# Performance work log

Hardware: AMD Instinct MI355X
Metric: run time of the kernel (lower is better)

Reference implementation:

```python
import jax, jax.numpy as jnp
import numpy as np

D = 512        # feat_dim
H_ENC = 8      # motion_encoder heads
H_SA = 4       # semantic-aware attention heads
BS, L, N = 8, 512, 4096
LN_EPS = 1e-5


def _layernorm(x, g, b):
    m = jnp.mean(x, axis=-1, keepdims=True)
    v = jnp.var(x, axis=-1, keepdims=True)
    return (x - m) * jax.lax.rsqrt(v + LN_EPS) * g + b


def _linear(x, w, b):
    # torch nn.Linear convention: w [out, in]
    return x @ w.T + b


def setup_inputs() -> dict:
    key = jax.random.key(0)
    ks = jax.random.split(key, 24)
    s = 0.02
    inp = {
        "motion": jax.random.normal(ks[0], (BS, L, D), jnp.float32),
        "scene_xyz": jax.random.normal(ks[1], (BS, N, 3), jnp.float32),
        "scene_feats": jax.random.normal(ks[2], (BS, N, D), jnp.float32),
        "spatial_prior": jax.random.normal(ks[3], (BS, L, N), jnp.float32),
        # motion_encoder (pre-norm MHA + pre-norm MLP, both residual)
        "enc_ln1_g": jnp.ones((D,), jnp.float32),
        "enc_ln1_b": jnp.zeros((D,), jnp.float32),
        "enc_qkv_w": jax.random.normal(ks[4], (3 * D, D), jnp.float32) * s,
        "enc_qkv_b": jnp.zeros((3 * D,), jnp.float32),
        "enc_out_w": jax.random.normal(ks[5], (D, D), jnp.float32) * s,
        "enc_out_b": jnp.zeros((D,), jnp.float32),
        "enc_ln2_g": jnp.ones((D,), jnp.float32),
        "enc_ln2_b": jnp.zeros((D,), jnp.float32),
        "enc_ff1_w": jax.random.normal(ks[6], (D, D), jnp.float32) * s,
        "enc_ff1_b": jnp.zeros((D,), jnp.float32),
        "enc_ff2_w": jax.random.normal(ks[7], (D, D), jnp.float32) * s,
        "enc_ff2_b": jnp.zeros((D,), jnp.float32),
        # SemanticAwareAttention
        "sa_q_w": jax.random.normal(ks[8], (D, D), jnp.float32) * s,
        "sa_q_b": jnp.zeros((D,), jnp.float32),
        "sa_kv_w": jax.random.normal(ks[9], (2 * D, D), jnp.float32) * s,
        "sa_kv_b": jnp.zeros((2 * D,), jnp.float32),
        "sa_out_w": jax.random.normal(ks[10], (D, D), jnp.float32) * s,
        "sa_out_b": jnp.zeros((D,), jnp.float32),
        # final concat-MLP: in 2D -> 4D -> D  (Mlp(2D, D, expansion=4))
        "mlp_fc1_w": jax.random.normal(ks[11], (4 * D, 2 * D), jnp.float32) * s,
        "mlp_fc1_b": jnp.zeros((4 * D,), jnp.float32),
        "mlp_fc2_w": jax.random.normal(ks[12], (D, 4 * D), jnp.float32) * s,
        "mlp_fc2_b": jnp.zeros((D,), jnp.float32),
    }
    return inp


def _forward(motion, scene_xyz, scene_feats, spatial_prior,
             enc_ln1_g, enc_ln1_b, enc_qkv_w, enc_qkv_b, enc_out_w, enc_out_b,
             enc_ln2_g, enc_ln2_b, enc_ff1_w, enc_ff1_b, enc_ff2_w, enc_ff2_b,
             sa_q_w, sa_q_b, sa_kv_w, sa_kv_b, sa_out_w, sa_out_b,
             mlp_fc1_w, mlp_fc1_b, mlp_fc2_w, mlp_fc2_b):
    bs, slen, _ = motion.shape
    n = scene_feats.shape[1]
    dh_enc = D // H_ENC
    dh_sa = D // H_SA

    # ---- motion encoder: pre-norm MHA + residual ----
    h = _layernorm(motion, enc_ln1_g, enc_ln1_b)
    qkv = _linear(h, enc_qkv_w, enc_qkv_b)                      # [bs, L, 3D]
    q, k, v = jnp.split(qkv, 3, axis=-1)
    q = q.reshape(bs, slen, H_ENC, dh_enc)
    k = k.reshape(bs, slen, H_ENC, dh_enc)
    v = v.reshape(bs, slen, H_ENC, dh_enc)
    att = jnp.einsum("bqhd,bkhd->bhqk", q, k) * (dh_enc ** -0.5)
    att = jax.nn.softmax(att, axis=-1)
    o = jnp.einsum("bhqk,bkhd->bqhd", att, v).reshape(bs, slen, D)
    x = motion + _linear(o, enc_out_w, enc_out_b)

    # ---- pre-norm MLP + residual ----
    h2 = _layernorm(x, enc_ln2_g, enc_ln2_b)
    ff = _linear(jax.nn.gelu(_linear(h2, enc_ff1_w, enc_ff1_b), approximate=False),
                 enc_ff2_w, enc_ff2_b)
    motion_sca = x + ff

    # ---- SemanticAwareAttention ----
    q = _linear(motion_sca, sa_q_w, sa_q_b) * (D ** -0.5)       # scale by feat_dim (faithful)
    kv = _linear(scene_feats, sa_kv_w, sa_kv_b)
    k, v = jnp.split(kv, 2, axis=-1)
    # faithful to torch: q.view(bs, H, L, d) splits heads from flattened (L, D)
    q = q.reshape(bs, H_SA, slen, dh_sa)
    k = k.reshape(bs, n, H_SA, dh_sa).transpose(0, 2, 1, 3)     # [bs, H, N, d]
    v = v.reshape(bs, n, H_SA, dh_sa).transpose(0, 2, 1, 3)
    att = jnp.einsum("bhqd,bhkd->bhqk", q, k) + spatial_prior[:, None, :, :]
    att = jax.nn.softmax(att, axis=-1)
    sm = jnp.einsum("bhqk,bhkd->bqhd", att, v).reshape(bs, slen, D)
    sm_feature = _linear(sm, sa_out_w, sa_out_b)

    # ---- concat + MLP ----
    cat = jnp.concatenate([motion_sca, sm_feature], axis=-1)    # [bs, L, 2D]
    out = _linear(jax.nn.gelu(_linear(cat, mlp_fc1_w, mlp_fc1_b), approximate=False),
                  mlp_fc2_w, mlp_fc2_b)
    return out


def reference(motion, scene_xyz, scene_feats, spatial_prior,
              enc_ln1_g, enc_ln1_b, enc_qkv_w, enc_qkv_b, enc_out_w, enc_out_b,
              enc_ln2_g, enc_ln2_b, enc_ff1_w, enc_ff1_b, enc_ff2_w, enc_ff2_b,
              sa_q_w, sa_q_b, sa_kv_w, sa_kv_b, sa_out_w, sa_out_b,
              mlp_fc1_w, mlp_fc1_b, mlp_fc2_w, mlp_fc2_b):
    return _forward(motion, scene_xyz, scene_feats, spatial_prior,
                    enc_ln1_g, enc_ln1_b, enc_qkv_w, enc_qkv_b, enc_out_w, enc_out_b,
                    enc_ln2_g, enc_ln2_b, enc_ff1_w, enc_ff1_b, enc_ff2_w, enc_ff2_b,
                    sa_q_w, sa_q_b, sa_kv_w, sa_kv_b, sa_out_w, sa_out_b,
                    mlp_fc1_w, mlp_fc1_b, mlp_fc2_w, mlp_fc2_b)
```

## Files before the change

### kernel.cpp

```cpp
#include <hip/hip_runtime.h>

typedef unsigned short bf16_t;
typedef __attribute__((ext_vector_type(8))) short bf16x8;
typedef __attribute__((ext_vector_type(4))) float f32x4;

__device__ __forceinline__ float bf2f(bf16_t u) {
  union { unsigned int i; float f; } v; v.i = ((unsigned int)u) << 16; return v.f;
}
__device__ __forceinline__ bf16_t f2bf(float f) {
  union { float f; unsigned int i; } v; v.f = f;
  unsigned int u = v.i;
  u += 0x7fffu + ((u >> 16) & 1u);
  return (bf16_t)(u >> 16);
}
__device__ __forceinline__ float gelu_exact(float x) {
  return 0.5f * x * (1.0f + erff(x * 0.7071067811865475f));
}
__device__ __forceinline__ void g2l16(bf16_t* l, const bf16_t* g) {
  __builtin_amdgcn_global_load_lds(
      (const __attribute__((address_space(1))) unsigned int*)g,
      (__attribute__((address_space(3))) unsigned int*)l, 16, 0, 0);
}

__global__ __launch_bounds__(256) void f2bf_kernel(const float4* __restrict__ s,
                                                   ushort4* __restrict__ d, int n4) {
  int i = blockIdx.x * 256 + threadIdx.x;
  if (i < n4) {
    float4 f = s[i];
    ushort4 u; u.x = f2bf(f.x); u.y = f2bf(f.y); u.z = f2bf(f.z); u.w = f2bf(f.w);
    d[i] = u;
  }
}

__global__ __launch_bounds__(256) void ln_kernel(const float* __restrict__ x,
                                                 const float* __restrict__ g,
                                                 const float* __restrict__ bta,
                                                 bf16_t* __restrict__ y) {
  const int w = threadIdx.x >> 6, lane = threadIdx.x & 63;
  const long row = (long)blockIdx.x * 4 + w;
  const long base = row * 512;
  const int c0 = lane << 2;
  float v[8];
  float4 f0 = *(const float4*)(x + base + c0);
  float4 f1 = *(const float4*)(x + base + 256 + c0);
  v[0]=f0.x; v[1]=f0.y; v[2]=f0.z; v[3]=f0.w;
  v[4]=f1.x; v[5]=f1.y; v[6]=f1.z; v[7]=f1.w;
  float s = 0.f;
#pragma unroll
  for (int c=0;c<8;++c) s += v[c];
#pragma unroll
  for (int o=32;o>0;o>>=1) s += __shfl_xor(s, o);
  const float mean = s * 0.001953125f;
  float ss = 0.f;
#pragma unroll
  for (int c=0;c<8;++c) { float d = v[c]-mean; ss += d*d; }
#pragma unroll
  for (int o=32;o>0;o>>=1) ss += __shfl_xor(ss, o);
  const float rstd = rsqrtf(ss * 0.001953125f + 1e-5f);
  ushort4 o0, o1;
  o0.x = f2bf((v[0]-mean)*rstd*g[c0+0] + bta[c0+0]);
  o0.y = f2bf((v[1]-mean)*rstd*g[c0+1] + bta[c0+1]);
  o0.z = f2bf((v[2]-mean)*rstd*g[c0+2] + bta[c0+2]);
  o0.w = f2bf((v[3]-mean)*rstd*g[c0+3] + bta[c0+3]);
  o1.x = f2bf((v[4]-mean)*rstd*g[256+c0+0] + bta[256+c0+0]);
  o1.y = f2bf((v[5]-mean)*rstd*g[256+c0+1] + bta[256+c0+1]);
  o1.z = f2bf((v[6]-mean)*rstd*g[256+c0+2] + bta[256+c0+2]);
  o1.w = f2bf((v[7]-mean)*rstd*g[256+c0+3] + bta[256+c0+3]);
  *(ushort4*)(y + base + c0) = o0;
  *(ushort4*)(y + base + 256 + c0) = o1;
}

struct MmaNT {
  const bf16_t* A; const bf16_t* W; const float* bias; const float* res; void* C;
  long lda, sAb, sAh;
  long ldw, sWb, sWh;
  long ldr, sRb, sRh;
  long ldc, sCb, sCh;
  int K, zdiv, cBf, act;
  float scale;
};

template <int MT>
__global__ __launch_bounds__(256) void mma_nt_kernel(MmaNT p) {
  constexpr int FM = MT / 32;
  constexpr int TILE_E = (MT + 128) * 32;
  constexpr int ST_E = MT * 128;
  constexpr int SM_E = (TILE_E > ST_E) ? TILE_E : ST_E;
  __shared__ __align__(16) bf16_t smem[SM_E];
  bf16_t* Al = smem;
  bf16_t* Wl = smem + MT * 32;
  const int tid = threadIdx.x;
  const int wid = tid >> 6, lane = tid & 63;
  const int wm = wid & 1, wn = wid >> 1;
  const int quad = lane >> 4, l16 = lane & 15;
  const int z = blockIdx.z;
  const int zb = z / p.zdiv, zh = z % p.zdiv;

  const int nbx = gridDim.x;
  const int nwg = nbx * gridDim.y;
  const int flat = blockIdx.y * nbx + blockIdx.x;
  const int sw = (flat & 7) * (nwg >> 3) + (flat >> 3);
  const int bx = sw % nbx, by = sw / nbx;

  const long m0 = (long)by * MT;
  const long n0 = (long)bx * 128;

  f32x4 zero4 = {0.f, 0.f, 0.f, 0.f};
  f32x4 acc[FM][4];
#pragma unroll
  for (int fm = 0; fm < FM; ++fm)
#pragma unroll
    for (int fn = 0; fn < 4; ++fn) acc[fm][fn] = zero4;

  if constexpr (MT == 128) {
    const bf16_t* Ag = p.A + (long)zb * p.sAb + (long)zh * p.sAh + m0 * p.lda;
    const bf16_t* Wg = p.W + (long)zb * p.sWb + (long)zh * p.sWh + n0 * p.ldw;
    const int sr = lane >> 2;
    const int sc = (lane & 3) * 8;
    for (int kc = 0; kc < p.K; kc += 32) {
#pragma unroll
      for (int j = 0; j < 2; ++j)
        g2l16(&Al[(j * 64 + wid * 16) * 32],
              Ag + (long)(j * 64 + wid * 16 + sr) * p.lda + kc + sc);
#pragma unroll
      for (int j = 0; j < 2; ++j)
        g2l16(&Wl[(j * 64 + wid * 16) * 32],
              Wg + (long)(j * 64 + wid * 16 + sr) * p.ldw + kc + sc);
      __syncthreads();
      bf16x8 af[FM], wf[4];
#pragma unroll
      for (int fm = 0; fm < FM; ++fm)
        af[fm] = *(const bf16x8*)&Al[(wm * 64 + fm * 16 + l16) * 32 + quad * 8];
#pragma unroll
      for (int fn = 0; fn < 4; ++fn)
        wf[fn] = *(const bf16x8*)&Wl[(wn * 64 + fn * 16 + l16) * 32 + quad * 8];
#pragma unroll
      for (int fm = 0; fm < FM; ++fm)
#pragma unroll
        for (int fn = 0; fn < 4; ++fn)
          acc[fm][fn] = __builtin_amdgcn_mfma_f32_16x16x32_bf16(af[fm], wf[fn], acc[fm][fn], 0, 0, 0);
      __syncthreads();
    }
  } else {
    const bf16_t* Ag = p.A + (long)zb * p.sAb + (long)zh * p.sAh +
                       (m0 + wm * (MT / 2) + l16) * p.lda;
    const bf16_t* Wg = p.W + (long)zb * p.sWb + (long)zh * p.sWh +
                       (n0 + wn * 64 + l16) * p.ldw;
    bf16x8 a0[FM], w0[4], a1[FM], w1[4], an0[FM], wn0[4], an1[FM], wn1[4];
#pragma unroll
    for (int fm = 0; fm < FM; ++fm) {
      a0[fm] = *(const bf16x8*)(Ag + (long)(fm * 16) * p.lda + quad * 8);
      a1[fm] = *(const bf16x8*)(Ag + (long)(fm * 16) * p.lda + 32 + quad * 8);
    }
#pragma unroll
    for (int fn = 0; fn < 4; ++fn) {
      w0[fn] = *(const bf16x8*)(Wg + (long)(fn * 16) * p.ldw + quad * 8);
      w1[fn] = *(const bf16x8*)(Wg + (long)(fn * 16) * p.ldw + 32 + quad * 8);
    }
    for (int kc = 0; kc < p.K; kc += 64) {
      int k2 = kc + 64;
      if (k2 > p.K - 64) k2 = p.K - 64;
#pragma unroll
      for (int fm = 0; fm < FM; ++fm)
        an0[fm] = *(const bf16x8*)(Ag + (long)(fm * 16) * p.lda + k2 + quad * 8);
#pragma unroll
      for (int fn = 0; fn < 4; ++fn)
        wn0[fn] = *(const bf16x8*)(Wg + (long)(fn * 16) * p.ldw + k2 + quad * 8);
#pragma unroll
      for (int fm = 0; fm < FM; ++fm)
#pragma unroll
        for (int fn = 0; fn < 4; ++fn)
          acc[fm][fn] = __builtin_amdgcn_mfma_f32_16x16x32_bf16(a0[fm], w0[fn], acc[fm][fn], 0, 0, 0);
#pragma unroll
      for (int fm = 0; fm < FM; ++fm)
        an1[fm] = *(const bf16x8*)(Ag + (long)(fm * 16) * p.lda + k2 + 32 + quad * 8);
#pragma unroll
      for (int fn = 0; fn < 4; ++fn)
        wn1[fn] = *(const bf16x8*)(Wg + (long)(fn * 16) * p.ldw + k2 + 32 + quad * 8);
#pragma unroll
      for (int fm = 0; fm < FM; ++fm)
#pragma unroll
        for (int fn = 0; fn < 4; ++fn)
          acc[fm][fn] = __builtin_amdgcn_mfma_f32_16x16x32_bf16(a1[fm], w1[fn], acc[fm][fn], 0, 0, 0);
#pragma unroll
      for (int fm = 0; fm < FM; ++fm) { a0[fm] = an0[fm]; a1[fm] = an1[fm]; }
#pragma unroll
      for (int fn = 0; fn < 4; ++fn) { w0[fn] = wn0[fn]; w1[fn] = wn1[fn]; }
    }
  }

  const long cOff = (long)zb * p.sCb + (long)zh * p.sCh;
  const long rOff = (long)zb * p.sRb + (long)zh * p.sRh;
  if (p.cBf) {
#pragma unroll
    for (int fm = 0; fm < FM; ++fm) {
#pragma unroll
      for (int fn = 0; fn < 4; ++fn) {
        const int lc = wn * 64 + fn * 16 + l16;
        const long col = n0 + lc;
        const float bv = p.bias ? p.bias[col] : 0.f;
#pragma unroll
        for (int r = 0; r < 4; ++r) {
          const int lr = wm * (MT / 2) + fm * 16 + quad * 4 + r;
          float t = acc[fm][fn][r] + bv;
          if (p.act) t = gelu_exact(t);
          t *= p.scale;
          if (p.res) t += p.res[rOff + (m0 + lr) * p.ldr + col];
          smem[lr * 128 + lc] = f2bf(t);
        }
      }
    }
    __syncthreads();
    bf16_t* Cg = (bf16_t*)p.C + cOff + m0 * p.ldc + n0;
#pragma unroll
    for (int i = 0; i < MT / 16; ++i) {
      const int flat2 = tid + i * 256;
      const int r = flat2 >> 4, c = (flat2 & 15) * 8;
      *(uint4*)(Cg + (long)r * p.ldc + c) = *(const uint4*)&smem[r * 128 + c];
    }
  } else {
#pragma unroll
    for (int fm = 0; fm < FM; ++fm) {
#pragma unroll
      for (int fn = 0; fn < 4; ++fn) {
        const long col = n0 + wn * 64 + fn * 16 + l16;
        const float bv = p.bias ? p.bias[col] : 0.f;
#pragma unroll
        for (int r = 0; r < 4; ++r) {
          const long row = m0 + wm * (MT / 2) + fm * 16 + quad * 4 + r;
          float t = acc[fm][fn][r] + bv;
          if (p.act) t = gelu_exact(t);
          t *= p.scale;
          if (p.res) t += p.res[rOff + row * p.ldr + col];
          ((float*)p.C)[cOff + row * p.ldc + col] = t;
        }
      }
    }
  }
}

struct TransP {
  const bf16_t* src; bf16_t* dst;
  long sSb, sSh, ld;
  int nh, N, D;
};

__global__ __launch_bounds__(256) void transpose_kernel(TransP p) {
  __shared__ bf16_t T[64][72];
  const int tid = threadIdx.x;
  const int z = blockIdx.z;
  const int zb = z / p.nh, zh = z % p.nh;
  const long n0 = (long)blockIdx.x * 64;
  const long d0 = (long)blockIdx.y * 64;
  const bf16_t* src = p.src + (long)zb * p.sSb + (long)zh * p.sSh;
  bf16_t* dst = p.dst + (long)z * p.D * p.N;
#pragma unroll
  for (int i = 0; i < 2; ++i) {
    int flat = tid + i * 256, r = flat >> 3, cg = flat & 7;
    uint4 v = *(const uint4*)(src + (n0 + r) * p.ld + d0 + cg * 8);
    *(uint4*)&T[r][cg * 8] = v;
  }
  __syncthreads();
#pragma unroll
  for (int i = 0; i < 2; ++i) {
    int flat = tid + i * 256, dr = flat >> 3, ncg = flat & 7;
    uint4 o;
    unsigned int* op = (unsigned int*)&o;
#pragma unroll
    for (int j = 0; j < 4; ++j)
      op[j] = (unsigned int)T[ncg * 8 + 2 * j][dr] | ((unsigned int)T[ncg * 8 + 2 * j + 1][dr] << 16);
    *(uint4*)(dst + (d0 + dr) * p.N + n0 + ncg * 8) = o;
  }
}

struct FlashP2 {
  const bf16_t* Q; const bf16_t* K; const bf16_t* VT; const float* prior;
  float* partO; float* partML;
  long ldq, sQb, sQh;
  long ldk, sKb, sKh;
  long sVz, sPb;
  int nh, N, segN;
  float scale;
};

template <int DH, int HASP>
__global__ __launch_bounds__(512) void flash3_kernel(FlashP2 p) {
  constexpr int KK = DH / 32;
  constexpr int NFO = DH / 16;
  constexpr int KE = 64 * DH;
  constexpr int VE = DH * 64;
  constexpr int PE = 128 * 72;
  __shared__ __align__(16) bf16_t smem[KE + VE + PE];
  bf16_t* Kl = smem;
  bf16_t* Vl = smem + KE;
  bf16_t* Pl = smem + KE + VE;
  const int tid = threadIdx.x;
  const int w = tid >> 6, lane = tid & 63;
  const int quad = lane >> 4, l16 = lane & 15;
  const int z = blockIdx.z;
  const int zb = z / p.nh, zh = z % p.nh;
  const int qr0 = blockIdx.y * 128 + w * 16;
  const bf16_t* Q = p.Q + (long)zb * p.sQb + (long)zh * p.sQh + (long)qr0 * p.ldq;
  const bf16_t* K = p.K + (long)zb * p.sKb + (long)zh * p.sKh;
  const bf16_t* VT = p.VT + (long)z * p.sVz;

  bf16x8 qf[KK];
#pragma unroll
  for (int kk = 0; kk < KK; ++kk)
    qf[kk] = *(const bf16x8*)(Q + (long)l16 * p.ldq + kk * 32 + quad * 8);

  f32x4 zero4 = {0.f, 0.f, 0.f, 0.f};
  f32x4 O[NFO];
  float m_[4], l_[4];
#pragma unroll
  for (int f = 0; f < NFO; ++f) O[f] = zero4;
#pragma unroll
  for (int r = 0; r < 4; ++r) { m_[r] = -1e30f; l_[r] = 0.f; }

  constexpr int LPR = DH / 8;
  constexpr int RPC = 512 / DH;
  constexpr int KCW = (64 / RPC) / 8;
  constexpr int VCW = (DH / 8) / 8;
  const int krl = lane / LPR;
  const int kcb = (lane % LPR) * 16;
  const int vrl = lane >> 3;
  const int vcb = (lane & 7) * 16;

  const float* PRrow = HASP ? (p.prior + (long)zb * p.sPb +
                               (long)(qr0 + quad * 4) * p.N) : (const float*)nullptr;

  const int k0 = blockIdx.x * p.segN;
  const int kend = k0 + p.segN;

  float pr0[4][4], pr1[4][4];
  if (HASP) {
#pragma unroll
    for (int nf = 0; nf < 4; ++nf)
#pragma unroll
      for (int r = 0; r < 4; ++r)
        pr0[nf][r] = PRrow[(long)r * p.N + k0 + nf * 16 + l16];
  }

  auto body = [&](int ktc, float (&prC)[4][4], float (&prN)[4][4]) {
    __syncthreads();
#pragma unroll
    for (int j = 0; j < KCW; ++j) {
      const int R0 = (w + 8 * j) * RPC;
      const int r = R0 + krl;
      const int cs = kcb ^ ((r & 7) << 4);
      g2l16(&Kl[R0 * DH], K + (long)(ktc + r) * p.ldk + (cs >> 1));
    }
#pragma unroll
    for (int j = 0; j < VCW; ++j) {
      const int R0 = (w + 8 * j) * 8;
      const int r = R0 + vrl;
      const int cs = vcb ^ ((r & 7) << 4);
      g2l16(&Vl[R0 * 64], VT + (long)r * p.N + ktc + (cs >> 1));
    }
    __syncthreads();
    if (HASP) {
      int kn = ktc + 64;
      if (kn > p.N - 64) kn = p.N - 64;
#pragma unroll
      for (int nf = 0; nf < 4; ++nf)
#pragma unroll
        for (int r = 0; r < 4; ++r)
          prN[nf][r] = PRrow[(long)r * p.N + kn + nf * 16 + l16];
    }
    f32x4 s[4];
#pragma unroll
    for (int nf = 0; nf < 4; ++nf) s[nf] = zero4;
    __builtin_amdgcn_s_setprio(1);
#pragma unroll
    for (int nf = 0; nf < 4; ++nf)
#pragma unroll
      for (int kk = 0; kk < KK; ++kk) {
        bf16x8 kf = *(const bf16x8*)&Kl[(nf * 16 + l16) * DH +
                                        ((kk * 32 + quad * 8) ^ ((l16 & 7) << 3))];
        s[nf] = __builtin_amdgcn_mfma_f32_16x16x32_bf16(qf[kk], kf, s[nf], 0, 0, 0);
      }
    __builtin_amdgcn_s_setprio(0);
    float tm[4];
#pragma unroll
    for (int r = 0; r < 4; ++r) tm[r] = -1e30f;
#pragma unroll
    for (int nf = 0; nf < 4; ++nf)
#pragma unroll
      for (int r = 0; r < 4; ++r) {
        float t = s[nf][r] * p.scale;
        if (HASP) t += prC[nf][r];
        s[nf][r] = t;
        tm[r] = fmaxf(tm[r], t);
      }
#pragma unroll
    for (int off = 1; off < 16; off <<= 1)
#pragma unroll
      for (int r = 0; r < 4; ++r) tm[r] = fmaxf(tm[r], __shfl_xor(tm[r], off));
    const int ok = (tm[0] <= m_[0] + 8.f) && (tm[1] <= m_[1] + 8.f) &&
                   (tm[2] <= m_[2] + 8.f) && (tm[3] <= m_[3] + 8.f);
    if (!__all(ok)) {
      float alpha[4];
#pragma unroll
      for (int r = 0; r < 4; ++r) {
        float mn = fmaxf(m_[r], tm[r]);
        alpha[r] = __expf(m_[r] - mn);
        m_[r] = mn;
        l_[r] *= alpha[r];
      }
#pragma unroll
      for (int f = 0; f < NFO; ++f)
#pragma unroll
        for (int r = 0; r < 4; ++r) O[f][r] *= alpha[r];
    }
    float rs[4];
#pragma unroll
    for (int r = 0; r < 4; ++r) rs[r] = 0.f;
#pragma unroll
    for (int nf = 0; nf < 4; ++nf)
#pragma unroll
      for (int r = 0; r < 4; ++r) {
        float pv = __expf(s[nf][r] - m_[r]);
        s[nf][r] = pv;
        rs[r] += pv;
      }
#pragma unroll
    for (int off = 1; off < 16; off <<= 1)
#pragma unroll
      for (int r = 0; r < 4; ++r) rs[r] += __shfl_xor(rs[r], off);
#pragma unroll
    for (int r = 0; r < 4; ++r) l_[r] += rs[r];
#pragma unroll
    for (int nf = 0; nf < 4; ++nf)
#pragma unroll
      for (int r = 0; r < 4; ++r)
        Pl[(w * 16 + quad * 4 + r) * 72 + nf * 16 + l16] = f2bf(s[nf][r]);
    bf16x8 pf[2];
#pragma unroll
    for (int kk2 = 0; kk2 < 2; ++kk2)
      pf[kk2] = *(const bf16x8*)&Pl[(w * 16 + l16) * 72 + kk2 * 32 + quad * 8];
    __builtin_amdgcn_s_setprio(1);
#pragma unroll
    for (int f = 0; f < NFO; ++f)
#pragma unroll
      for (int kk2 = 0; kk2 < 2; ++kk2) {
        bf16x8 vf = *(const bf16x8*)&Vl[(f * 16 + l16) * 64 +
                                        ((kk2 * 32 + quad * 8) ^ ((l16 & 7) << 3))];
        O[f] = __builtin_amdgcn_mfma_f32_16x16x32_bf16(pf[kk2], vf, O[f], 0, 0, 0);
      }
    __builtin_amdgcn_s_setprio(0);
  };

  for (int kt = k0; kt < kend; kt += 128) {
    body(kt, pr0, pr1);
    body(kt + 64, pr1, pr0);
  }

  const long t = ((long)z * gridDim.y + blockIdx.y) * gridDim.x + blockIdx.x;
  float* PO = p.partO + t * (128 * DH);
  float* PM = p.partML + t * 256;
  const int row = w * 16 + quad * 4;
#pragma unroll
  for (int f = 0; f < NFO; ++f)
#pragma unroll
    for (int r = 0; r < 4; ++r)
      PO[(long)(row + r) * DH + f * 16 + l16] = O[f][r];
  if (l16 == 0) {
#pragma unroll
    for (int r = 0; r < 4; ++r) {
      PM[(row + r) * 2 + 0] = m_[r];
      PM[(row + r) * 2 + 1] = l_[r];
    }
  }
}

struct MergeP {
  const float* partO; const float* partML; bf16_t* C;
  long ldc, sCb;
  int nh, y;
};

template <int DH, int NS>
__global__ __launch_bounds__(256) void fmerge_kernel(MergeP p) {
  const int tid = threadIdx.x;
  const int r = tid >> 1, ch = tid & 1;
  const int blk = blockIdx.x;
  const int z = blk / p.y, qb = blk % p.y;
  const int zb = z / p.nh, zh = z % p.nh;
  const long t0 = (long)blk * NS;
  float mm[NS], wgt[NS];
  float mstar = -1e30f;
#pragma unroll
  for (int s = 0; s < NS; ++s) {
    mm[s] = p.partML[(t0 + s) * 256 + r * 2];
    mstar = fmaxf(mstar, mm[s]);
  }
  float lsum = 0.f;
#pragma unroll
  for (int s = 0; s < NS; ++s) {
    wgt[s] = __expf(mm[s] - mstar);
    lsum += wgt[s] * p.partML[(t0 + s) * 256 + r * 2 + 1];
  }
  const float inv = 1.0f / lsum;
  const int c0 = ch * (DH / 2);
  bf16_t* Cp = p.C + (long)zb * p.sCb + (long)(qb * 128 + r) * p.ldc + (long)zh * DH + c0;
#pragma unroll
  for (int c = 0; c < DH / 2; c += 4) {
    float4 acc = make_float4(0.f, 0.f, 0.f, 0.f);
#pragma unroll
    for (int s = 0; s < NS; ++s) {
      float4 v = *(const float4*)(p.partO + (t0 + s) * (128 * DH) + (long)r * DH + c0 + c);
      acc.x += wgt[s] * v.x; acc.y += wgt[s] * v.y;
      acc.z += wgt[s] * v.z; acc.w += wgt[s] * v.w;
    }
    ushort4 o;
    o.x = f2bf(acc.x * inv); o.y = f2bf(acc.y * inv);
    o.z = f2bf(acc.z * inv); o.w = f2bf(acc.w * inv);
    *(ushort4*)(Cp + c) = o;
  }
}

#define MB(x) ((long)(x) << 20)

extern "C" void kernel_launch(void* const* d_in, const int* in_sizes, int n_in,
                              void* d_out, int out_size, void* d_ws, size_t ws_size,
                              hipStream_t stream) {
  const float* motion      = (const float*)d_in[0];
  const float* scene_feats = (const float*)d_in[2];
  const float* prior       = (const float*)d_in[3];
  const float* ln1_g = (const float*)d_in[4];
  const float* ln1_b = (const float*)d_in[5];
  const float* qkv_w = (const float*)d_in[6];
  const float* qkv_b = (const float*)d_in[7];
  const float* out_w = (const float*)d_in[8];
  const float* out_b = (const float*)d_in[9];
  const float* ln2_g = (const float*)d_in[10];
  const float* ln2_b = (const float*)d_in[11];
  const float* ff1_w = (const float*)d_in[12];
  const float* ff1_b = (const float*)d_in[13];
  const float* ff2_w = (const float*)d_in[14];
  const float* ff2_b = (const float*)d_in[15];
  const float* saq_w = (const float*)d_in[16];
  const float* saq_b = (const float*)d_in[17];
  const float* sakv_w = (const float*)d_in[18];
  const float* sakv_b = (const float*)d_in[19];
  const float* saout_w = (const float*)d_in[20];
  const float* saout_b = (const float*)d_in[21];
  const float* fc1_w = (const float*)d_in[22];
  const float* fc1_b = (const float*)d_in[23];
  const float* fc2_w = (const float*)d_in[24];
  const float* fc2_b = (const float*)d_in[25];

  char* W = (char*)d_ws;
  bf16_t* h_bf    = (bf16_t*)(W + MB(0));
  float*  x_f     = (float*) (W + MB(4));
  bf16_t* o_ff    = (bf16_t*)(W + MB(12));
  bf16_t* qkv_bf  = (bf16_t*)(W + MB(16));
  bf16_t* qsa     = (bf16_t*)(W + MB(28));
  bf16_t* sm_bf   = (bf16_t*)(W + MB(32));
  bf16_t* cat_bf  = (bf16_t*)(W + MB(36));
  bf16_t* fc1g    = (bf16_t*)(W + MB(44));
  bf16_t* vTe     = (bf16_t*)(W + MB(60));
  bf16_t* kv_bf   = (bf16_t*)(W + MB(64));
  bf16_t* vT      = (bf16_t*)(W + MB(128));
  bf16_t* wbase   = (bf16_t*)(W + MB(160));
  bf16_t* scene_bf= (bf16_t*)(W + MB(172));

  float* encO  = (float*)fc1g;
  float* encML = (float*)cat_bf;
  float* saO   = (float*)scene_bf;
  float* saML  = (float*)vTe;

  bf16_t* wq   = wbase + 0L;
  bf16_t* wout = wbase + 786432L;
  bf16_t* wff1 = wbase + 1048576L;
  bf16_t* wff2 = wbase + 1310720L;
  bf16_t* wsaq = wbase + 1572864L;
  bf16_t* wskv = wbase + 1835008L;
  bf16_t* wsout= wbase + 2359296L;
  bf16_t* wfc1 = wbase + 2621440L;
  bf16_t* wfc2 = wbase + 4718592L;

  const dim3 B256(256);
  const dim3 B512(512);
  auto cvt = [&](const float* s, bf16_t* d, long n) {
    int n4 = (int)(n / 4);
    f2bf_kernel<<<(n4 + 255) / 256, B256, 0, stream>>>((const float4*)s, (ushort4*)d, n4);
  };
  cvt(qkv_w,  wq,   786432);
  cvt(out_w,  wout, 262144);
  cvt(ff1_w,  wff1, 262144);
  cvt(ff2_w,  wff2, 262144);
  cvt(saq_w,  wsaq, 262144);
  cvt(sakv_w, wskv, 524288);
  cvt(saout_w,wsout,262144);
  cvt(fc1_w,  wfc1, 2097152);
  cvt(fc2_w,  wfc2, 1048576);
  cvt(scene_feats, scene_bf, 16777216);

  ln_kernel<<<1024, B256, 0, stream>>>(motion, ln1_g, ln1_b, h_bf);

  { MmaNT p{}; p.scale=1.f; p.zdiv=1; p.cBf=1;
    p.A=h_bf; p.lda=512; p.W=wq; p.ldw=512; p.bias=qkv_b;
    p.C=qkv_bf; p.ldc=1536; p.K=512;
    mma_nt_kernel<128><<<dim3(12,32,1), B256, 0, stream>>>(p); }

  { TransP t{}; t.src=qkv_bf+1024; t.dst=vTe; t.sSb=786432; t.sSh=64;
    t.ld=1536; t.nh=8; t.N=512; t.D=64;
    transpose_kernel<<<dim3(8,1,64), B256, 0, stream>>>(t); }
  { FlashP2 p{};
    p.Q=qkv_bf;     p.ldq=1536; p.sQb=786432; p.sQh=64;
    p.K=qkv_bf+512; p.ldk=1536; p.sKb=786432; p.sKh=64;
    p.VT=vTe; p.sVz=32768;
    p.prior=nullptr; p.sPb=0;
    p.partO=encO; p.partML=encML;
    p.nh=8; p.N=512; p.segN=256; p.scale=0.125f;
    flash3_kernel<64,0><<<dim3(2,4,64), B512, 0, stream>>>(p); }
  { MergeP m{}; m.partO=encO; m.partML=encML; m.C=o_ff;
    m.ldc=512; m.sCb=262144; m.nh=8; m.y=4;
    fmerge_kernel<64,2><<<256, B256, 0, stream>>>(m); }

  { MmaNT p{}; p.scale=1.f; p.zdiv=1;
    p.A=o_ff; p.lda=512; p.W=wout; p.ldw=512; p.bias=out_b;
    p.res=motion; p.ldr=512;
    p.C=x_f; p.ldc=512; p.K=512;
    mma_nt_kernel<64><<<dim3(4,64,1), B256, 0, stream>>>(p); }

  ln_kernel<<<1024, B256, 0, stream>>>(x_f, ln2_g, ln2_b, h_bf);

  { MmaNT p{}; p.scale=1.f; p.zdiv=1; p.cBf=1; p.act=1;
    p.A=h_bf; p.lda=512; p.W=wff1; p.ldw=512; p.bias=ff1_b;
    p.C=o_ff; p.ldc=512; p.K=512;
    mma_nt_kernel<64><<<dim3(4,64,1), B256, 0, stream>>>(p); }

  { MmaNT p{}; p.scale=1.f; p.zdiv=1; p.cBf=1;
    p.A=o_ff; p.lda=512; p.W=wff2; p.ldw=512; p.bias=ff2_b;
    p.res=x_f; p.ldr=512;
    p.C=cat_bf; p.ldc=1024; p.K=512;
    mma_nt_kernel<64><<<dim3(4,64,1), B256, 0, stream>>>(p); }

  { MmaNT p{}; p.zdiv=1; p.cBf=1; p.scale=0.04419417382415922f;
    p.A=cat_bf; p.lda=1024; p.W=wsaq; p.ldw=512; p.bias=saq_b;
    p.C=qsa; p.ldc=512; p.K=512;
    mma_nt_kernel<64><<<dim3(4,64,1), B256, 0, stream>>>(p); }

  { MmaNT p{}; p.scale=1.f; p.zdiv=1; p.cBf=1;
    p.A=scene_bf; p.lda=512; p.W=wskv; p.ldw=512; p.bias=sakv_b;
    p.C=kv_bf; p.ldc=1024; p.K=512;
    mma_nt_kernel<128><<<dim3(8,256,1), B256, 0, stream>>>(p); }

  { TransP t{}; t.src=kv_bf+512; t.dst=vT; t.sSb=4194304; t.sSh=128;
    t.ld=1024; t.nh=4; t.N=4096; t.D=128;
    transpose_kernel<<<dim3(64,2,32), B256, 0, stream>>>(t); }
  { FlashP2 p{};
    p.Q=qsa;   p.ldq=128;  p.sQb=262144;  p.sQh=65536;
    p.K=kv_bf; p.ldk=1024; p.sKb=4194304; p.sKh=128;
    p.VT=vT; p.sVz=524288;
    p.prior=prior; p.sPb=2097152;
    p.partO=saO; p.partML=saML;
    p.nh=4; p.N=4096; p.segN=1024; p.scale=1.f;
    flash3_kernel<128,1><<<dim3(4,4,32), B512, 0, stream>>>(p); }
  { MergeP m{}; m.partO=saO; m.partML=saML; m.C=sm_bf;
    m.ldc=512; m.sCb=262144; m.nh=4; m.y=4;
    fmerge_kernel<128,4><<<128, B256, 0, stream>>>(m); }

  { MmaNT p{}; p.scale=1.f; p.zdiv=1; p.cBf=1;
    p.A=sm_bf; p.lda=512; p.W=wsout; p.ldw=512; p.bias=saout_b;
    p.C=cat_bf + 512; p.ldc=1024; p.K=512;
    mma_nt_kernel<64><<<dim3(4,64,1), B256, 0, stream>>>(p); }

  { MmaNT p{}; p.scale=1.f; p.zdiv=1; p.cBf=1; p.act=1;
    p.A=cat_bf; p.lda=1024; p.W=wfc1; p.ldw=1024; p.bias=fc1_b;
    p.C=fc1g; p.ldc=2048; p.K=1024;
    mma_nt_kernel<128><<<dim3(16,32,1), B256, 0, stream>>>(p); }

  { MmaNT p{}; p.scale=1.f; p.zdiv=1;
    p.A=fc1g; p.lda=2048; p.W=wfc2; p.ldw=2048; p.bias=fc2_b;
    p.C=d_out; p.ldc=512; p.K=2048;
    mma_nt_kernel<64><<<dim3(4,64,1), B256, 0, stream>>>(p); }
}
```

Baseline: 658.5 us.

## Double-buffer K/V LDS tiles in flash attention to overlap loads with compute

Splits the K and V shared-memory tiles into two buffers. The next 64-key tile is staged with async global-to-LDS loads, along with its prior values, while MFMA work runs on the current tile. This cuts the per-tile pair of barriers down to one, and the s_setprio hints around the MFMA loops are dropped. In exchange the kernel roughly doubles its K/V LDS footprint, which may lower the number of resident blocks per CU.

```diff
diff --git a/kernel.cpp b/kernel.cpp
--- a/kernel.cpp
+++ b/kernel.cpp
@@ -290,10 +290,12 @@
   constexpr int KE = 64 * DH;
   constexpr int VE = DH * 64;
   constexpr int PE = 128 * 72;
-  __shared__ __align__(16) bf16_t smem[KE + VE + PE];
-  bf16_t* Kl = smem;
-  bf16_t* Vl = smem + KE;
-  bf16_t* Pl = smem + KE + VE;
+  __shared__ __align__(16) bf16_t smem[2 * KE + 2 * VE + PE];
+  bf16_t* Kl0 = smem;
+  bf16_t* Kl1 = smem + KE;
+  bf16_t* Vl0 = smem + 2 * KE;
+  bf16_t* Vl1 = smem + 2 * KE + VE;
+  bf16_t* Pl  = smem + 2 * KE + 2 * VE;
   const int tid = threadIdx.x;
   const int w = tid >> 6, lane = tid & 63;
   const int quad = lane >> 4, l16 = lane & 15;
@@ -332,17 +334,7 @@
   const int k0 = blockIdx.x * p.segN;
   const int kend = k0 + p.segN;
 
-  float pr0[4][4], pr1[4][4];
-  if (HASP) {
-#pragma unroll
-    for (int nf = 0; nf < 4; ++nf)
-#pragma unroll
-      for (int r = 0; r < 4; ++r)
-        pr0[nf][r] = PRrow[(long)r * p.N + k0 + nf * 16 + l16];
-  }
-
-  auto body = [&](int ktc, float (&prC)[4][4], float (&prN)[4][4]) {
-    __syncthreads();
+  auto stage = [&](bf16_t* Kl, bf16_t* Vl, int ktc) {
 #pragma unroll
     for (int j = 0; j < KCW; ++j) {
       const int R0 = (w + 8 * j) * RPC;
@@ -357,20 +349,21 @@
       const int cs = vcb ^ ((r & 7) << 4);
       g2l16(&Vl[R0 * 64], VT + (long)r * p.N + ktc + (cs >> 1));
     }
-    __syncthreads();
-    if (HASP) {
-      int kn = ktc + 64;
-      if (kn > p.N - 64) kn = p.N - 64;
-#pragma unroll
-      for (int nf = 0; nf < 4; ++nf)
-#pragma unroll
-        for (int r = 0; r < 4; ++r)
-          prN[nf][r] = PRrow[(long)r * p.N + kn + nf * 16 + l16];
-    }
+  };
+
+  auto loadprior = [&](int kn, float (&dst)[4][4]) {
+    if (kn > p.N - 64) kn = p.N - 64;
+#pragma unroll
+    for (int nf = 0; nf < 4; ++nf)
+#pragma unroll
+      for (int r = 0; r < 4; ++r)
+        dst[nf][r] = PRrow[(long)r * p.N + kn + nf * 16 + l16];
+  };
+
+  auto body = [&](const bf16_t* Kl, const bf16_t* Vl, float (&prC)[4][4]) {
     f32x4 s[4];
 #pragma unroll
     for (int nf = 0; nf < 4; ++nf) s[nf] = zero4;
-    __builtin_amdgcn_s_setprio(1);
 #pragma unroll
     for (int nf = 0; nf < 4; ++nf)
 #pragma unroll
@@ -379,7 +372,6 @@
                                         ((kk * 32 + quad * 8) ^ ((l16 & 7) << 3))];
         s[nf] = __builtin_amdgcn_mfma_f32_16x16x32_bf16(qf[kk], kf, s[nf], 0, 0, 0);
       }
-    __builtin_amdgcn_s_setprio(0);
     float tm[4];
 #pragma unroll
     for (int r = 0; r < 4; ++r) tm[r] = -1e30f;
@@ -438,7 +430,6 @@
 #pragma unroll
     for (int kk2 = 0; kk2 < 2; ++kk2)
       pf[kk2] = *(const bf16x8*)&Pl[(w * 16 + l16) * 72 + kk2 * 32 + quad * 8];
-    __builtin_amdgcn_s_setprio(1);
 #pragma unroll
     for (int f = 0; f < NFO; ++f)
 #pragma unroll
@@ -447,12 +438,22 @@
                                         ((kk2 * 32 + quad * 8) ^ ((l16 & 7) << 3))];
         O[f] = __builtin_amdgcn_mfma_f32_16x16x32_bf16(pf[kk2], vf, O[f], 0, 0, 0);
       }
-    __builtin_amdgcn_s_setprio(0);
   };
 
+  float pr0[4][4], pr1[4][4];
+  stage(Kl0, Vl0, k0);
+  if (HASP) loadprior(k0, pr0);
+  __syncthreads();
+
   for (int kt = k0; kt < kend; kt += 128) {
-    body(kt, pr0, pr1);
-    body(kt + 64, pr1, pr0);
+    stage(Kl1, Vl1, kt + 64);
+    if (HASP) loadprior(kt + 64, pr1);
+    body(Kl0, Vl0, pr0);
+    __syncthreads();
+    if (kt + 128 < kend) stage(Kl0, Vl0, kt + 128);
+    if (HASP) loadprior(kt + 128, pr0);
+    body(Kl1, Vl1, pr1);
+    __syncthreads();
   }
 
   const long t = ((long)z * gridDim.y + blockIdx.y) * gridDim.x + blockIdx.x;
```

Result: no change. 648.9 us (-1.5%).
